# Kernel optimization log

Hardware: AMD Instinct MI355X
Metric: run time of the kernel (lower is better)

## Reference

```python
import jax, jax.numpy as jnp
import numpy as np

NUM_USERS = 100000
NUM_RECIPES = 200000
EMB = 32
RDIM = 96
D = EMB + RDIM  # 128, shared node feature dim
E = 1500000
NUM_LAYERS = 3


def setup_inputs() -> dict:
    key = jax.random.key(0)
    k1, k2, k3, k4, k5, k6 = jax.random.split(key, 6)
    usr_emb = 0.1 * jax.random.normal(k1, (NUM_USERS, D), jnp.float32)      # usr_embedding.weight (init std=0.1)
    rcp_emb = 0.1 * jax.random.normal(k2, (NUM_RECIPES, EMB), jnp.float32)  # rcp_embedding.weight
    recipe_feat = jax.random.normal(k3, (NUM_RECIPES, RDIM), jnp.float32)   # x_dict['recipe']
    user_idx = jax.random.randint(k4, (E,), 0, NUM_USERS, jnp.int32)        # edge_index row 0 (user)
    rcp_idx = jax.random.randint(k5, (E,), 0, NUM_RECIPES, jnp.int32)       # edge_index row 1 (recipe)
    edge_weight = 1.0 + 4.0 * jax.random.uniform(k6, (E,), jnp.float32)     # review scores in [1,5]
    return {"usr_emb": usr_emb, "rcp_emb": rcp_emb, "recipe_feat": recipe_feat,
            "edge_weight": edge_weight, "user_idx": user_idx, "rcp_idx": rcp_idx}


def reference(usr_emb, rcp_emb, recipe_feat, edge_weight, user_idx, rcp_idx):
    seg = jax.ops.segment_sum
    alpha = 1.0 / (NUM_LAYERS + 1)

    # LightGCN symmetric normalization with review-score edge weights
    # (HeteroLGConv: msg = x_src[src] * w / sqrt(deg_w(src) * deg_w(dst)); sum-aggregate at dst).
    deg_u = seg(edge_weight, user_idx, num_segments=NUM_USERS)    # weighted user degree
    deg_r = seg(edge_weight, rcp_idx, num_segments=NUM_RECIPES)   # weighted recipe degree
    norm = edge_weight * jax.lax.rsqrt(jnp.clip(deg_u[user_idx] * deg_r[rcp_idx], 1e-12, None))  # [E]

    rcp_x = jnp.concatenate([rcp_emb, recipe_feat], axis=1)  # [R, D]
    usr_x = usr_emb                                           # [U, D]
    rec_out = rcp_x * alpha
    usr_out = usr_x * alpha

    for _ in range(NUM_LAYERS):
        # user -> recipe propagation
        rcp_x = seg(usr_x[user_idx] * norm[:, None], rcp_idx, num_segments=NUM_RECIPES)
        rec_out = rec_out + rcp_x * alpha
        # recipe -> user propagation (reverse edges)
        usr_x = seg(rcp_x[rcp_idx] * norm[:, None], user_idx, num_segments=NUM_USERS)
        usr_out = usr_out + usr_x * alpha

    return usr_out, rec_out
```

## Files before the change

### kernel.cpp

```cpp
#include <hip/hip_runtime.h>
#include <hip/hip_fp16.h>


typedef unsigned long long ull;

constexpr int NU   = 100000;
constexpr int NR   = 200000;
constexpr int EMB  = 32;
constexpr int RDIM = 96;
constexpr int D    = 128;
constexpr int NE   = 1500000;
constexpr float ALPHA = 0.25f;

constexpr ull DEG_MASK = (1ULL << 44) - 1;
constexpr float DEG_SCALE = 1048576.0f;
constexpr float DEG_INV   = 1.0f / 1048576.0f;

constexpr int NBK    = 391;
constexpr int SPAN_R = 512;
constexpr int SPAN_U = 256;
constexpr int EPB    = 4096;
constexpr int B1     = (NE + EPB - 1) / EPB;
constexpr int CB     = (NU * D / 16 + 255) / 256;


__device__ __forceinline__ unsigned pack_bf16x2(float x, float y) {
    unsigned ux = __float_as_uint(x);
    unsigned uy = __float_as_uint(y);
    ux += 0x7fffu + ((ux >> 16) & 1u);
    uy += 0x7fffu + ((uy >> 16) & 1u);
    return (ux >> 16) | (uy & 0xffff0000u);
}

__device__ __forceinline__ float blo(unsigned u) { return __uint_as_float(u << 16); }
__device__ __forceinline__ float bhi(unsigned u) { return __uint_as_float(u & 0xffff0000u); }


__global__ void hist_kernel(const int* __restrict__ ui,
                            const int* __restrict__ ri,
                            unsigned* __restrict__ hist_u,
                            unsigned* __restrict__ hist_r,
                            const float4* __restrict__ usr_emb4,
                            uint4* __restrict__ emb_h4) {
    if ((int)blockIdx.x >= B1) {
        int t = ((int)blockIdx.x - B1) * 256 + threadIdx.x;
        if (t < NU * D / 16) {
            int base = t * 4;
            float4 a = usr_emb4[base], b = usr_emb4[base + 1];
            float4 c = usr_emb4[base + 2], d = usr_emb4[base + 3];
            uint4 o0 = {pack_bf16x2(a.x, a.y), pack_bf16x2(a.z, a.w),
                        pack_bf16x2(b.x, b.y), pack_bf16x2(b.z, b.w)};
            uint4 o1 = {pack_bf16x2(c.x, c.y), pack_bf16x2(c.z, c.w),
                        pack_bf16x2(d.x, d.y), pack_bf16x2(d.z, d.w)};
            emb_h4[t * 2]     = o0;
            emb_h4[t * 2 + 1] = o1;
        }
        return;
    }
    __shared__ unsigned hu[NBK], hr[NBK];
    for (int j = threadIdx.x; j < NBK; j += 256) { hu[j] = 0; hr[j] = 0; }
    __syncthreads();
    int base = blockIdx.x * EPB;
    for (int k = 0; k < 16; ++k) {
        int i = base + k * 256 + threadIdx.x;
        if (i < NE) {
            atomicAdd(&hu[ui[i] >> 8], 1u);
            atomicAdd(&hr[ri[i] >> 9], 1u);
        }
    }
    __syncthreads();
    for (int j = threadIdx.x; j < NBK; j += 256) {
        hist_u[j * B1 + blockIdx.x] = hu[j];
        hist_r[j * B1 + blockIdx.x] = hr[j];
    }
}


__global__ void scan_hist(unsigned* __restrict__ hist_r,
                          unsigned* __restrict__ hist_u,
                          unsigned* __restrict__ btot) {
    __shared__ unsigned tmp[512];
    bool isR = (int)blockIdx.x < NBK;
    int j = isR ? (int)blockIdx.x : (int)blockIdx.x - NBK;
    unsigned* h = (isR ? hist_r : hist_u) + (size_t)j * B1;
    int i = threadIdx.x;
    unsigned v = (i < B1) ? h[i] : 0;
    tmp[i] = v;
    __syncthreads();
    for (int o = 1; o < 512; o <<= 1) {
        unsigned t = (i >= o) ? tmp[i - o] : 0;
        __syncthreads();
        tmp[i] += t;
        __syncthreads();
    }
    if (i < B1) h[i] = tmp[i] - v;
    if (i == 511) btot[blockIdx.x] = tmp[511];
}


__global__ void scan_btot(const unsigned* __restrict__ btot,
                          unsigned* __restrict__ boff_r,
                          unsigned* __restrict__ boff_u) {
    __shared__ unsigned tmp[512];
    bool isR = (blockIdx.x == 0);
    unsigned* boff = isR ? boff_r : boff_u;
    int i = threadIdx.x;
    unsigned v = (i < NBK) ? btot[(isR ? 0 : NBK) + i] : 0;
    tmp[i] = v;
    __syncthreads();
    for (int o = 1; o < 512; o <<= 1) {
        unsigned t = (i >= o) ? tmp[i - o] : 0;
        __syncthreads();
        tmp[i] += t;
        __syncthreads();
    }
    if (i < NBK) boff[i] = tmp[i] - v;
    if (i == 0) boff[NBK] = tmp[511];
}


__global__ void scatter_kernel(const int* __restrict__ ui,
                               const int* __restrict__ ri,
                               const float* __restrict__ w,
                               const unsigned* __restrict__ hist_u,
                               const unsigned* __restrict__ hist_r,
                               const unsigned* __restrict__ boff_u,
                               const unsigned* __restrict__ boff_r,
                               ull* __restrict__ buf_u,
                               ull* __restrict__ buf_r) {
    __shared__ unsigned cu[NBK], cr[NBK];
    for (int j = threadIdx.x; j < NBK; j += 256) {
        cu[j] = boff_u[j] + hist_u[j * B1 + blockIdx.x];
        cr[j] = boff_r[j] + hist_r[j * B1 + blockIdx.x];
    }
    __syncthreads();
    int base = blockIdx.x * EPB;
    for (int k = 0; k < 16; ++k) {
        int i = base + k * 256 + threadIdx.x;
        if (i < NE) {
            int u = ui[i], r = ri[i];
            ull wh = (ull)__half_as_ushort(__float2half(w[i]));
            ull rec_r = (ull)(unsigned)u | ((ull)(r & 511) << 18) | (wh << 32);
            ull rec_u = (ull)(unsigned)r | ((ull)(u & 255) << 18) | (wh << 32);
            unsigned sr = atomicAdd(&cr[r >> 9], 1u);
            unsigned su = atomicAdd(&cu[u >> 8], 1u);
            buf_r[sr] = rec_r;
            buf_u[su] = rec_u;
        }
    }
}


__global__ void count_kernel(const ull* __restrict__ buf_r,
                             const ull* __restrict__ buf_u,
                             const unsigned* __restrict__ boff_r,
                             const unsigned* __restrict__ boff_u,
                             ull* __restrict__ pk_r,
                             ull* __restrict__ pk_u) {
    bool isR = (int)blockIdx.x < NBK;
    int j = isR ? (int)blockIdx.x : (int)blockIdx.x - NBK;
    const ull* buf = isR ? buf_r : buf_u;
    const unsigned* boff = isR ? boff_r : boff_u;
    ull* pk = isR ? pk_r : pk_u;
    int span = isR ? SPAN_R : SPAN_U;
    int nnode = isR ? NR : NU;
    __shared__ unsigned cnt[512], wfx[512];
    for (int i = threadIdx.x; i < span; i += 256) { cnt[i] = 0; wfx[i] = 0; }
    __syncthreads();
    unsigned beg = boff[j], end = boff[j + 1];
    for (unsigned e = beg + threadIdx.x; e < end; e += 256) {
        ull rec = buf[e];
        int dlow = (int)((rec >> 18) & 511);
        float wv = __half2float(__ushort_as_half((unsigned short)(rec >> 32)));
        atomicAdd(&cnt[dlow], 1u);
        atomicAdd(&wfx[dlow], (unsigned)(wv * DEG_SCALE + 0.5f));
    }
    __syncthreads();
    int nb = j * span;
    for (int i = threadIdx.x; i < span; i += 256) {
        int node = nb + i;
        if (node < nnode) pk[node] = ((ull)cnt[i] << 44) | (ull)wfx[i];
    }
}


__global__ void scan_block_both(const ull* __restrict__ pk_r,
                                const ull* __restrict__ pk_u,
                                int* __restrict__ rp_r,
                                int* __restrict__ rp_u,
                                int* __restrict__ bsum, int nbR) {
    __shared__ int tmp[256];
    bool isR = (int)blockIdx.x < nbR;
    const ull* pk = isR ? pk_r : pk_u;
    int* excl = isR ? rp_r : rp_u;
    int ncnt  = isR ? NR : NU;
    int b     = isR ? (int)blockIdx.x : (int)blockIdx.x - nbR;
    int nscan = ncnt + 1;
    int i = b * 256 + threadIdx.x;
    int v = 0;
    if (i < ncnt) v = ((int)(pk[i] >> 44) + 7) & ~7;
    tmp[threadIdx.x] = v;
    __syncthreads();
    for (int off = 1; off < 256; off <<= 1) {
        int t = (threadIdx.x >= off) ? tmp[threadIdx.x - off] : 0;
        __syncthreads();
        tmp[threadIdx.x] += t;
        __syncthreads();
    }
    if (i < nscan) excl[i] = tmp[threadIdx.x] - v;
    if (threadIdx.x == 255) bsum[blockIdx.x] = tmp[255];
}

__global__ void scan_bsum2(int* __restrict__ bsum, int nbR, int nbU) {
    __shared__ int tmp[1024];
    int off = (blockIdx.x == 0) ? 0 : nbR;
    int nb  = (blockIdx.x == 0) ? nbR : nbU;
    int i = threadIdx.x;
    int v = (i < nb) ? bsum[off + i] : 0;
    tmp[i] = v;
    __syncthreads();
    for (int o = 1; o < 1024; o <<= 1) {
        int t = (i >= o) ? tmp[i - o] : 0;
        __syncthreads();
        tmp[i] += t;
        __syncthreads();
    }
    if (i < nb) bsum[off + i] = tmp[i] - v;
}

__global__ void finalize_both(const int* __restrict__ rp_r,
                              const int* __restrict__ rp_u,
                              const ull* __restrict__ pk_r,
                              const ull* __restrict__ pk_u,
                              int2* __restrict__ combo_r,
                              int2* __restrict__ combo_u,
                              const int* __restrict__ bsum, int nbR) {
    bool isR = (int)blockIdx.x < nbR;
    const int* rp = isR ? rp_r : rp_u;
    const ull* pk = isR ? pk_r : pk_u;
    int2* combo   = isR ? combo_r : combo_u;
    int ncnt  = isR ? NR : NU;
    int b     = isR ? (int)blockIdx.x : (int)blockIdx.x - nbR;
    int i = b * 256 + threadIdx.x;
    if (i < ncnt + 1) {
        int rpv = rp[i] + bsum[blockIdx.x];
        float deg = (i < ncnt) ? (float)(pk[i] & DEG_MASK) * DEG_INV : 0.0f;
        combo[i] = make_int2(rpv, __float_as_int(deg));
    }
}


__global__ void emit_kernel(const ull* __restrict__ buf_r,
                            const ull* __restrict__ buf_u,
                            const unsigned* __restrict__ boff_r,
                            const unsigned* __restrict__ boff_u,
                            const int2* __restrict__ combo_r,
                            const int2* __restrict__ combo_u,
                            unsigned* __restrict__ pair_r,
                            unsigned* __restrict__ pair_u) {
    bool isR = (int)blockIdx.x < NBK;
    int j = isR ? (int)blockIdx.x : (int)blockIdx.x - NBK;
    const ull* buf = isR ? buf_r : buf_u;
    const unsigned* boff = isR ? boff_r : boff_u;
    const int2* combo  = isR ? combo_r : combo_u;
    const int2* comboO = isR ? combo_u : combo_r;
    unsigned* pair = isR ? pair_r : pair_u;
    int span = isR ? SPAN_R : SPAN_U;
    int nnode = isR ? NR : NU;
    __shared__ int rp_l[512];
    __shared__ float deg_l[512];
    __shared__ unsigned cur[512];
    int nb = j * span;
    for (int i = threadIdx.x; i < span; i += 256) {
        int node = nb + i;
        int2 c = (node < nnode) ? combo[node] : make_int2(0, 0);
        rp_l[i] = c.x;
        deg_l[i] = __int_as_float(c.y);
        cur[i] = 0;
    }
    __syncthreads();
    unsigned beg = boff[j], end = boff[j + 1];
    for (unsigned e = beg + threadIdx.x; e < end; e += 256) {
        ull rec = buf[e];
        unsigned src = (unsigned)(rec & 0x3FFFFu);
        int dlow = (int)((rec >> 18) & 511);
        float wv = __half2float(__ushort_as_half((unsigned short)(rec >> 32)));
        float dO = __int_as_float(comboO[src].y);
        float nv = wv * rsqrtf(fmaxf(deg_l[dlow] * dO, 1e-12f));
        unsigned short hb = __half_as_ushort(__float2half(nv));
        unsigned n14 = ((unsigned)hb + 1u) >> 1;
        unsigned rank = atomicAdd(&cur[dlow], 1u);
        pair[rp_l[dlow] + (int)rank] = (n14 << 18) | src;
    }
}


__global__ void gather_rows(const unsigned* __restrict__ src,
                            const int2* __restrict__ combo,
                            const unsigned* __restrict__ pair,
                            unsigned* __restrict__ xout,
                            float* __restrict__ out_f,
                            const unsigned* __restrict__ prev1,
                            const unsigned* __restrict__ prev2,
                            const float* __restrict__ init_a,
                            const float* __restrict__ init_b,
                            int nrows) {
    int wid  = (blockIdx.x * blockDim.x + threadIdx.x) >> 6;
    wid = __builtin_amdgcn_readfirstlane(wid);
    int lane = threadIdx.x & 63;
    if (wid >= nrows) return;

    int beg = __builtin_amdgcn_readfirstlane(combo[wid].x);
    int end = __builtin_amdgcn_readfirstlane(combo[wid + 1].x);
    float x0 = 0.f, y0 = 0.f, x1 = 0.f, y1 = 0.f;
    float x2 = 0.f, y2 = 0.f, x3 = 0.f, y3 = 0.f;

#define LOAD_EDGE(P, AX, AY)                                                  \
    {                                                                         \
        unsigned s = (P) & 0x3FFFFu;                                          \
        float n = __half2float(__ushort_as_half(                              \
                      (unsigned short)(((P) >> 18) << 1)));                   \
        unsigned v = src[(size_t)s * 64 + lane];                              \
        AX += n * __uint_as_float(v << 16);                                   \
        AY += n * __uint_as_float(v & 0xffff0000u);                           \
    }

    int e = beg;
    for (; e + 16 <= end; e += 16) {
        uint4 pa = *reinterpret_cast<const uint4*>(pair + e);
        uint4 pb = *reinterpret_cast<const uint4*>(pair + e + 4);
        uint4 pc = *reinterpret_cast<const uint4*>(pair + e + 8);
        uint4 pd = *reinterpret_cast<const uint4*>(pair + e + 12);
        LOAD_EDGE(pa.x, x0, y0) LOAD_EDGE(pa.y, x1, y1)
        LOAD_EDGE(pa.z, x2, y2) LOAD_EDGE(pa.w, x3, y3)
        LOAD_EDGE(pb.x, x0, y0) LOAD_EDGE(pb.y, x1, y1)
        LOAD_EDGE(pb.z, x2, y2) LOAD_EDGE(pb.w, x3, y3)
        LOAD_EDGE(pc.x, x0, y0) LOAD_EDGE(pc.y, x1, y1)
        LOAD_EDGE(pc.z, x2, y2) LOAD_EDGE(pc.w, x3, y3)
        LOAD_EDGE(pd.x, x0, y0) LOAD_EDGE(pd.y, x1, y1)
        LOAD_EDGE(pd.z, x2, y2) LOAD_EDGE(pd.w, x3, y3)
    }
    for (; e < end; e += 8) {
        uint4 pa = *reinterpret_cast<const uint4*>(pair + e);
        uint4 pb = *reinterpret_cast<const uint4*>(pair + e + 4);
        LOAD_EDGE(pa.x, x0, y0) LOAD_EDGE(pa.y, x1, y1)
        LOAD_EDGE(pa.z, x2, y2) LOAD_EDGE(pa.w, x3, y3)
        LOAD_EDGE(pb.x, x0, y0) LOAD_EDGE(pb.y, x1, y1)
        LOAD_EDGE(pb.z, x2, y2) LOAD_EDGE(pb.w, x3, y3)
    }
#undef LOAD_EDGE

    x0 = (x0 + x1) + (x2 + x3);
    y0 = (y0 + y1) + (y2 + y3);

    size_t xo = (size_t)wid * 64 + lane;
    if (xout) xout[xo] = pack_bf16x2(x0, y0);

    if (out_f) {
        size_t o = (size_t)wid * D + lane * 2;
        float2 b;
        if (init_b) {
            b = (lane < 16)
                ? *reinterpret_cast<const float2*>(init_a + (size_t)wid * EMB + lane * 2)
                : *reinterpret_cast<const float2*>(init_b + (size_t)wid * RDIM + (lane * 2 - EMB));
        } else {
            b = *reinterpret_cast<const float2*>(init_a + o);
        }
        if (prev1) {
            unsigned v1 = prev1[xo], v2 = prev2[xo];
            float lo = b.x + blo(v1) + blo(v2) + x0;
            float hi = b.y + bhi(v1) + bhi(v2) + y0;
            float2 ov = {ALPHA * lo, ALPHA * hi};
            *reinterpret_cast<float2*>(out_f + o) = ov;
        } else {
            float2 ov = {ALPHA * (b.x + x0), ALPHA * (b.y + y0)};
            *reinterpret_cast<float2*>(out_f + o) = ov;
        }
    }
}

__global__ void gather_rows_acc(const unsigned* __restrict__ src,
                                const int2* __restrict__ combo,
                                const unsigned* __restrict__ pair,
                                unsigned* __restrict__ xout,
                                float* __restrict__ out_f,
                                int nrows) {
    int wid  = (blockIdx.x * blockDim.x + threadIdx.x) >> 6;
    wid = __builtin_amdgcn_readfirstlane(wid);
    int lane = threadIdx.x & 63;
    if (wid >= nrows) return;
    int beg = __builtin_amdgcn_readfirstlane(combo[wid].x);
    int end = __builtin_amdgcn_readfirstlane(combo[wid + 1].x);
    float x0 = 0.f, y0 = 0.f;
    for (int e = beg; e < end; ++e) {
        unsigned P = pair[e];
        unsigned s = P & 0x3FFFFu;
        float n = __half2float(__ushort_as_half((unsigned short)((P >> 18) << 1)));
        unsigned v = src[(size_t)s * 64 + lane];
        x0 += n * blo(v); y0 += n * bhi(v);
    }
    size_t xo = (size_t)wid * 64 + lane;
    if (xout) xout[xo] = pack_bf16x2(x0, y0);
    size_t o = (size_t)wid * D + lane * 2;
    float2 ov = *reinterpret_cast<float2*>(out_f + o);
    ov.x += ALPHA * x0; ov.y += ALPHA * y0;
    *reinterpret_cast<float2*>(out_f + o) = ov;
}

__global__ void init_out_kernel(const float* __restrict__ usr_emb,
                                const float* __restrict__ rcp_emb,
                                const float* __restrict__ rfeat,
                                float* __restrict__ out) {
    long long i = blockIdx.x * (long long)blockDim.x + threadIdx.x;
    const long long UD = (long long)NU * D;
    const long long RD = (long long)NR * D;
    if (i < UD) {
        out[i] = ALPHA * usr_emb[i];
    } else if (i < UD + RD) {
        long long j = i - UD;
        int r = (int)(j >> 7);
        int d = (int)(j & 127);
        float v = (d < EMB) ? rcp_emb[(long long)r * EMB + d]
                            : rfeat[(long long)r * RDIM + (d - EMB)];
        out[i] = ALPHA * v;
    }
}


extern "C" void kernel_launch(void* const* d_in, const int* in_sizes, int n_in,
                              void* d_out, int out_size, void* d_ws, size_t ws_size,
                              hipStream_t stream) {
    const float* usr_emb = (const float*)d_in[0];
    const float* rcp_emb = (const float*)d_in[1];
    const float* rfeat   = (const float*)d_in[2];
    const float* w       = (const float*)d_in[3];
    const int*   ui      = (const int*)d_in[4];
    const int*   ri      = (const int*)d_in[5];

    float* out     = (float*)d_out;
    float* usr_out = out;
    float* rec_out = out + (size_t)NU * D;

    char* p0 = (char*)d_ws;
    char* p = p0;
    auto take = [&](size_t bytes) -> char* {
        char* q = p;
        p += (bytes + 255) & ~(size_t)255;
        return q;
    };

    const int PR_SLOTS = NE + 7 * NR + 16;
    const int PU_SLOTS = NE + 7 * NU + 16;

    unsigned* pair_r = (unsigned*)take((size_t)PR_SLOTS * 4);
    unsigned* pair_u = (unsigned*)take((size_t)PU_SLOTS * 4);
    char*     zero_end = p;
    ull*      pk_u    = (ull*)take((size_t)NU * 8);
    ull*      pk_r    = (ull*)take((size_t)NR * 8);
    int*      rp_r    = (int*)take((size_t)(NR + 1) * 4);
    int*      rp_u    = (int*)take((size_t)(NU + 1) * 4);
    int2*     combo_r = (int2*)take((size_t)(NR + 1) * 8);
    int2*     combo_u = (int2*)take((size_t)(NU + 1) * 8);
    int*      bsum    = (int*)take(4096 * 4);
    unsigned* btot    = (unsigned*)take((size_t)2 * NBK * 4);
    unsigned* boff_r  = (unsigned*)take((size_t)(NBK + 1) * 4);
    unsigned* boff_u  = (unsigned*)take((size_t)(NBK + 1) * 4);
    unsigned* emb_h   = (unsigned*)take((size_t)NU * 64 * 4);

    const size_t xr_b = (size_t)NR * 64 * 4;
    const size_t xu_b = (size_t)NU * 64 * 4;
    size_t used_head = (size_t)(p - p0);
    bool deferred = (ws_size >= used_head + 3 * ((xr_b + 255) & ~(size_t)255)
                                         + 2 * ((xu_b + 255) & ~(size_t)255));

    unsigned *xr0, *xr1, *xr2, *xu0, *xu1;
    if (deferred) {
        xr0 = (unsigned*)take(xr_b); xr1 = (unsigned*)take(xr_b); xr2 = (unsigned*)take(xr_b);
        xu0 = (unsigned*)take(xu_b); xu1 = (unsigned*)take(xu_b);
    } else {
        xr0 = xr1 = xr2 = (unsigned*)take(xr_b);
        xu0 = xu1 = (unsigned*)take(xu_b);
    }

    ull*      buf_r  = (ull*)xr0;
    ull*      buf_u  = buf_r + NE;
    unsigned* hist_r = (unsigned*)(buf_u + NE);
    unsigned* hist_u = hist_r + (size_t)NBK * B1;

    const int B = 256;

    hipMemsetAsync(pair_r, 0, (size_t)(zero_end - (char*)pair_r), stream);

    hist_kernel<<<B1 + CB, B, 0, stream>>>(ui, ri, hist_u, hist_r,
                                           (const float4*)usr_emb, (uint4*)emb_h);
    scan_hist<<<2 * NBK, 512, 0, stream>>>(hist_r, hist_u, btot);
    scan_btot<<<2, 512, 0, stream>>>(btot, boff_r, boff_u);
    scatter_kernel<<<B1, B, 0, stream>>>(ui, ri, w, hist_u, hist_r,
                                         boff_u, boff_r, buf_u, buf_r);
    count_kernel<<<2 * NBK, B, 0, stream>>>(buf_r, buf_u, boff_r, boff_u, pk_r, pk_u);

    const int nbR = (NR + 1 + 255) / 256;
    const int nbU = (NU + 1 + 255) / 256;
    scan_block_both<<<nbR + nbU, 256, 0, stream>>>(pk_r, pk_u, rp_r, rp_u, bsum, nbR);
    scan_bsum2<<<2, 1024, 0, stream>>>(bsum, nbR, nbU);
    finalize_both<<<nbR + nbU, 256, 0, stream>>>(rp_r, rp_u, pk_r, pk_u,
                                                 combo_r, combo_u, bsum, nbR);
    emit_kernel<<<2 * NBK, B, 0, stream>>>(buf_r, buf_u, boff_r, boff_u,
                                           combo_r, combo_u, pair_r, pair_u);

    const int GB_R = (NR * 64 + B - 1) / B;
    const int GB_U = (NU * 64 + B - 1) / B;

    if (deferred) {
        gather_rows<<<GB_R, B, 0, stream>>>(emb_h, combo_r, pair_r, xr0,
                                            nullptr, nullptr, nullptr, nullptr, nullptr, NR);
        gather_rows<<<GB_U, B, 0, stream>>>(xr0, combo_u, pair_u, xu0,
                                            nullptr, nullptr, nullptr, nullptr, nullptr, NU);
        gather_rows<<<GB_R, B, 0, stream>>>(xu0, combo_r, pair_r, xr1,
                                            nullptr, nullptr, nullptr, nullptr, nullptr, NR);
        gather_rows<<<GB_U, B, 0, stream>>>(xr1, combo_u, pair_u, xu1,
                                            nullptr, nullptr, nullptr, nullptr, nullptr, NU);
        gather_rows<<<GB_R, B, 0, stream>>>(xu1, combo_r, pair_r, xr2,
                                            rec_out, xr0, xr1, rcp_emb, rfeat, NR);
        gather_rows<<<GB_U, B, 0, stream>>>(xr2, combo_u, pair_u, nullptr,
                                            usr_out, xu0, xu1, usr_emb, nullptr, NU);
    } else {
        long long tot = (long long)(NU + NR) * D;
        init_out_kernel<<<(int)((tot + B - 1) / B), B, 0, stream>>>(usr_emb, rcp_emb, rfeat, out);
        gather_rows_acc<<<GB_R, B, 0, stream>>>(emb_h, combo_r, pair_r, xr0, rec_out, NR);
        gather_rows_acc<<<GB_U, B, 0, stream>>>(xr0, combo_u, pair_u, xu0, usr_out, NU);
        gather_rows_acc<<<GB_R, B, 0, stream>>>(xu0, combo_r, pair_r, xr0, rec_out, NR);
        gather_rows_acc<<<GB_U, B, 0, stream>>>(xr0, combo_u, pair_u, xu0, usr_out, NU);
        gather_rows_acc<<<GB_R, B, 0, stream>>>(xu0, combo_r, pair_r, xr0, rec_out, NR);
        gather_rows_acc<<<GB_U, B, 0, stream>>>(xr0, combo_u, pair_u, nullptr, usr_out, NU);
    }
}
```

Measured before the change: 558.0 us.

## Pad CSR rows to 4, use nontemporal loads/stores, read user init from bf16 copy

Row padding in the pair arrays drops from multiples of 8 to multiples of 4, and a 4-edge tail step is added to the gather loop. The change aims to cut wasted padded-edge work and pair-array bytes. Pair-index loads, output stores and prev-layer reads become nontemporal to reduce cache pollution. The final user-output kernel now reads the initial embedding from the bf16 copy (emb_h) instead of fp32 usr_emb, which halves those bytes but lowers the precision of the residual term.

```diff
diff --git a/kernel.cpp b/kernel.cpp
--- a/kernel.cpp
+++ b/kernel.cpp
@@ -3,6 +3,8 @@
 
 
 typedef unsigned long long ull;
+typedef unsigned uint4v __attribute__((ext_vector_type(4)));
+typedef float float2v __attribute__((ext_vector_type(2)));
 
 constexpr int NU   = 100000;
 constexpr int NR   = 200000;
@@ -97,7 +99,6 @@
     if (i == 511) btot[blockIdx.x] = tmp[511];
 }
 
-
 __global__ void scan_btot(const unsigned* __restrict__ btot,
                           unsigned* __restrict__ boff_r,
                           unsigned* __restrict__ boff_u) {
@@ -198,7 +199,7 @@
     int nscan = ncnt + 1;
     int i = b * 256 + threadIdx.x;
     int v = 0;
-    if (i < ncnt) v = ((int)(pk[i] >> 44) + 7) & ~7;
+    if (i < ncnt) v = ((int)(pk[i] >> 44) + 3) & ~3;
     tmp[threadIdx.x] = v;
     __syncthreads();
     for (int off = 1; off < 256; off <<= 1) {
@@ -295,6 +296,7 @@
 }
 
 
+template<int IMODE>
 __global__ void gather_rows(const unsigned* __restrict__ src,
                             const int2* __restrict__ combo,
                             const unsigned* __restrict__ pair,
@@ -304,6 +306,7 @@
                             const unsigned* __restrict__ prev2,
                             const float* __restrict__ init_a,
                             const float* __restrict__ init_b,
+                            const unsigned* __restrict__ init_h,
                             int nrows) {
     int wid  = (blockIdx.x * blockDim.x + threadIdx.x) >> 6;
     wid = __builtin_amdgcn_readfirstlane(wid);
@@ -315,6 +318,7 @@
     float x0 = 0.f, y0 = 0.f, x1 = 0.f, y1 = 0.f;
     float x2 = 0.f, y2 = 0.f, x3 = 0.f, y3 = 0.f;
 
+#define PLOAD(E) __builtin_nontemporal_load(reinterpret_cast<const uint4v*>(pair + (E)))
 #define LOAD_EDGE(P, AX, AY)                                                  \
     {                                                                         \
         unsigned s = (P) & 0x3FFFFu;                                          \
@@ -327,55 +331,57 @@
 
     int e = beg;
     for (; e + 16 <= end; e += 16) {
-        uint4 pa = *reinterpret_cast<const uint4*>(pair + e);
-        uint4 pb = *reinterpret_cast<const uint4*>(pair + e + 4);
-        uint4 pc = *reinterpret_cast<const uint4*>(pair + e + 8);
-        uint4 pd = *reinterpret_cast<const uint4*>(pair + e + 12);
-        LOAD_EDGE(pa.x, x0, y0) LOAD_EDGE(pa.y, x1, y1)
-        LOAD_EDGE(pa.z, x2, y2) LOAD_EDGE(pa.w, x3, y3)
-        LOAD_EDGE(pb.x, x0, y0) LOAD_EDGE(pb.y, x1, y1)
-        LOAD_EDGE(pb.z, x2, y2) LOAD_EDGE(pb.w, x3, y3)
-        LOAD_EDGE(pc.x, x0, y0) LOAD_EDGE(pc.y, x1, y1)
-        LOAD_EDGE(pc.z, x2, y2) LOAD_EDGE(pc.w, x3, y3)
-        LOAD_EDGE(pd.x, x0, y0) LOAD_EDGE(pd.y, x1, y1)
-        LOAD_EDGE(pd.z, x2, y2) LOAD_EDGE(pd.w, x3, y3)
-    }
-    for (; e < end; e += 8) {
-        uint4 pa = *reinterpret_cast<const uint4*>(pair + e);
-        uint4 pb = *reinterpret_cast<const uint4*>(pair + e + 4);
-        LOAD_EDGE(pa.x, x0, y0) LOAD_EDGE(pa.y, x1, y1)
-        LOAD_EDGE(pa.z, x2, y2) LOAD_EDGE(pa.w, x3, y3)
-        LOAD_EDGE(pb.x, x0, y0) LOAD_EDGE(pb.y, x1, y1)
-        LOAD_EDGE(pb.z, x2, y2) LOAD_EDGE(pb.w, x3, y3)
+        uint4v pa = PLOAD(e), pb = PLOAD(e + 4), pc = PLOAD(e + 8), pd = PLOAD(e + 12);
+        LOAD_EDGE(pa[0], x0, y0) LOAD_EDGE(pa[1], x1, y1)
+        LOAD_EDGE(pa[2], x2, y2) LOAD_EDGE(pa[3], x3, y3)
+        LOAD_EDGE(pb[0], x0, y0) LOAD_EDGE(pb[1], x1, y1)
+        LOAD_EDGE(pb[2], x2, y2) LOAD_EDGE(pb[3], x3, y3)
+        LOAD_EDGE(pc[0], x0, y0) LOAD_EDGE(pc[1], x1, y1)
+        LOAD_EDGE(pc[2], x2, y2) LOAD_EDGE(pc[3], x3, y3)
+        LOAD_EDGE(pd[0], x0, y0) LOAD_EDGE(pd[1], x1, y1)
+        LOAD_EDGE(pd[2], x2, y2) LOAD_EDGE(pd[3], x3, y3)
+    }
+    for (; e + 8 <= end; e += 8) {
+        uint4v pa = PLOAD(e), pb = PLOAD(e + 4);
+        LOAD_EDGE(pa[0], x0, y0) LOAD_EDGE(pa[1], x1, y1)
+        LOAD_EDGE(pa[2], x2, y2) LOAD_EDGE(pa[3], x3, y3)
+        LOAD_EDGE(pb[0], x0, y0) LOAD_EDGE(pb[1], x1, y1)
+        LOAD_EDGE(pb[2], x2, y2) LOAD_EDGE(pb[3], x3, y3)
+    }
+    if (e < end) {
+        uint4v pa = PLOAD(e);
+        LOAD_EDGE(pa[0], x0, y0) LOAD_EDGE(pa[1], x1, y1)
+        LOAD_EDGE(pa[2], x2, y2) LOAD_EDGE(pa[3], x3, y3)
     }
 #undef LOAD_EDGE
+#undef PLOAD
 
     x0 = (x0 + x1) + (x2 + x3);
     y0 = (y0 + y1) + (y2 + y3);
 
     size_t xo = (size_t)wid * 64 + lane;
-    if (xout) xout[xo] = pack_bf16x2(x0, y0);
+    if (xout) __builtin_nontemporal_store(pack_bf16x2(x0, y0), &xout[xo]);
 
     if (out_f) {
         size_t o = (size_t)wid * D + lane * 2;
-        float2 b;
-        if (init_b) {
-            b = (lane < 16)
-                ? *reinterpret_cast<const float2*>(init_a + (size_t)wid * EMB + lane * 2)
-                : *reinterpret_cast<const float2*>(init_b + (size_t)wid * RDIM + (lane * 2 - EMB));
+        float bx, by;
+        if constexpr (IMODE == 1) {
+            float2v b = (lane < 16)
+                ? __builtin_nontemporal_load(reinterpret_cast<const float2v*>(
+                      init_a + (size_t)wid * EMB + lane * 2))
+                : __builtin_nontemporal_load(reinterpret_cast<const float2v*>(
+                      init_b + (size_t)wid * RDIM + (lane * 2 - EMB)));
+            bx = b[0]; by = b[1];
         } else {
-            b = *reinterpret_cast<const float2*>(init_a + o);
+            unsigned hv = __builtin_nontemporal_load(&init_h[xo]);
+            bx = blo(hv); by = bhi(hv);
         }
-        if (prev1) {
-            unsigned v1 = prev1[xo], v2 = prev2[xo];
-            float lo = b.x + blo(v1) + blo(v2) + x0;
-            float hi = b.y + bhi(v1) + bhi(v2) + y0;
-            float2 ov = {ALPHA * lo, ALPHA * hi};
-            *reinterpret_cast<float2*>(out_f + o) = ov;
-        } else {
-            float2 ov = {ALPHA * (b.x + x0), ALPHA * (b.y + y0)};
-            *reinterpret_cast<float2*>(out_f + o) = ov;
-        }
+        unsigned v1 = __builtin_nontemporal_load(&prev1[xo]);
+        unsigned v2 = __builtin_nontemporal_load(&prev2[xo]);
+        float lo = bx + blo(v1) + blo(v2) + x0;
+        float hi = by + bhi(v1) + bhi(v2) + y0;
+        float2v ov = {ALPHA * lo, ALPHA * hi};
+        __builtin_nontemporal_store(ov, reinterpret_cast<float2v*>(out_f + o));
     }
 }
 
@@ -449,8 +455,8 @@
         return q;
     };
 
-    const int PR_SLOTS = NE + 7 * NR + 16;
-    const int PU_SLOTS = NE + 7 * NU + 16;
+    const int PR_SLOTS = NE + 3 * NR + 16;
+    const int PU_SLOTS = NE + 3 * NU + 16;
 
     unsigned* pair_r = (unsigned*)take((size_t)PR_SLOTS * 4);
     unsigned* pair_u = (unsigned*)take((size_t)PU_SLOTS * 4);
@@ -512,18 +518,18 @@
     const int GB_U = (NU * 64 + B - 1) / B;
 
     if (deferred) {
-        gather_rows<<<GB_R, B, 0, stream>>>(emb_h, combo_r, pair_r, xr0,
-                                            nullptr, nullptr, nullptr, nullptr, nullptr, NR);
-        gather_rows<<<GB_U, B, 0, stream>>>(xr0, combo_u, pair_u, xu0,
-                                            nullptr, nullptr, nullptr, nullptr, nullptr, NU);
-        gather_rows<<<GB_R, B, 0, stream>>>(xu0, combo_r, pair_r, xr1,
-                                            nullptr, nullptr, nullptr, nullptr, nullptr, NR);
-        gather_rows<<<GB_U, B, 0, stream>>>(xr1, combo_u, pair_u, xu1,
-                                            nullptr, nullptr, nullptr, nullptr, nullptr, NU);
-        gather_rows<<<GB_R, B, 0, stream>>>(xu1, combo_r, pair_r, xr2,
-                                            rec_out, xr0, xr1, rcp_emb, rfeat, NR);
-        gather_rows<<<GB_U, B, 0, stream>>>(xr2, combo_u, pair_u, nullptr,
-                                            usr_out, xu0, xu1, usr_emb, nullptr, NU);
+        gather_rows<0><<<GB_R, B, 0, stream>>>(emb_h, combo_r, pair_r, xr0,
+                                               nullptr, nullptr, nullptr, nullptr, nullptr, nullptr, NR);
+        gather_rows<0><<<GB_U, B, 0, stream>>>(xr0, combo_u, pair_u, xu0,
+                                               nullptr, nullptr, nullptr, nullptr, nullptr, nullptr, NU);
+        gather_rows<0><<<GB_R, B, 0, stream>>>(xu0, combo_r, pair_r, xr1,
+                                               nullptr, nullptr, nullptr, nullptr, nullptr, nullptr, NR);
+        gather_rows<0><<<GB_U, B, 0, stream>>>(xr1, combo_u, pair_u, xu1,
+                                               nullptr, nullptr, nullptr, nullptr, nullptr, nullptr, NU);
+        gather_rows<1><<<GB_R, B, 0, stream>>>(xu1, combo_r, pair_r, xr2,
+                                               rec_out, xr0, xr1, rcp_emb, rfeat, nullptr, NR);
+        gather_rows<2><<<GB_U, B, 0, stream>>>(xr2, combo_u, pair_u, nullptr,
+                                               usr_out, xu0, xu1, nullptr, nullptr, emb_h, NU);
     } else {
         long long tot = (long long)(NU + NR) * D;
         init_out_kernel<<<(int)((tot + B - 1) / B), B, 0, stream>>>(usr_emb, rcp_emb, rfeat, out);
```

Result: faster. 529.3 us, median of 2 (-5.1%).
